# Optimization experiments

Hardware: AMD Instinct MI355X
Metric: run time of the kernel (lower is better)

Reference implementation:

```python
import jax, jax.numpy as jnp
import numpy as np

VOCAB = 50001; W2V = 300; S2V = 256; HID = 256; COUT = 256; NTAG = 4; NHEADS = 5
N_POSTS = 2048; SEQ = 64


def mha(x, wqkv, bqkv, wo, bo, h):
    # torch nn.MultiheadAttention (batch_first, eval mode, no mask)
    n, s, d = x.shape
    hd = d // h
    qkv = x @ wqkv.T + bqkv                      # [n, s, 3d]
    q, k, v = jnp.split(qkv, 3, axis=-1)
    rs = lambda t: t.reshape(n, s, h, hd).transpose(0, 2, 1, 3)  # [n, h, s, hd]
    q, k, v = rs(q), rs(k), rs(v)
    att = jax.nn.softmax(jnp.einsum('nhqd,nhkd->nhqk', q, k) * (hd ** -0.5), axis=-1)
    o = jnp.einsum('nhqk,nhkd->nhqd', att, v).transpose(0, 2, 1, 3).reshape(n, s, d)
    return o @ wo.T + bo


def gcn_conv(x, ei, w, b):
    n = x.shape[0]
    loops = jnp.arange(n)
    src = jnp.concatenate([ei[0], loops])
    dst = jnp.concatenate([ei[1], loops])
    deg = jax.ops.segment_sum(jnp.ones(dst.shape[0], dtype=x.dtype), dst, num_segments=n)
    dinv = jnp.where(deg > 0, jax.lax.rsqrt(deg), 0.0)
    norm = dinv[src] * dinv[dst]                 # [E+n]
    h = x @ w.T                                  # [n, out]
    return jax.ops.segment_sum(norm[:, None] * h[src], dst, num_segments=n) + b


def gcn_branch(x, ei, root, w1, b1, w2, b2):
    # GCN.forward: conv1 -> cat root feat -> relu -> conv2 -> relu -> cat conv1 root -> mean
    n = x.shape[0]
    c1 = gcn_conv(x, ei, w1, b1)                 # [n, HID]
    post_root = jnp.broadcast_to(x[root], (n, x.shape[1]))
    c2_in = jax.nn.relu(jnp.concatenate([c1, post_root], axis=1))
    c2 = jax.nn.relu(gcn_conv(c2_in, ei, w2, b2))
    c1_root = jnp.broadcast_to(c1[root], (n, c1.shape[1]))
    feat = jnp.concatenate([c1_root, c2], axis=1)  # [n, HID+COUT]
    return jnp.mean(feat, axis=0).reshape(1, -1)


def setup_inputs() -> dict:
    key = jax.random.key(0)
    ks = jax.random.split(key, 16)
    p = lambda i, shp, sc=0.02: jax.random.normal(ks[i], shp, dtype=jnp.float32) * sc
    return {
        'nodeText': jax.random.randint(ks[0], (N_POSTS, SEQ), 0, VOCAB),
        'edgeIndexTD': jax.random.randint(ks[1], (2, N_POSTS - 1), 0, N_POSTS),
        'edgeIndexBU': jax.random.randint(ks[2], (2, N_POSTS - 1), 0, N_POSTS),
        'threadIndex': 0,
        'mission': 1,
        'embed_w': p(3, (VOCAB, W2V), 1.0),
        'in_proj_w': p(4, (3 * W2V, W2V)),
        'in_proj_b': jnp.zeros((3 * W2V,), jnp.float32),
        'out_proj_w': p(5, (W2V, W2V)),
        'out_proj_b': jnp.zeros((W2V,), jnp.float32),
        's2v_w': p(6, (S2V, W2V)),
        's2v_b': jnp.zeros((S2V,), jnp.float32),
        'td_w1': p(7, (HID, S2V)), 'td_b1': jnp.zeros((HID,), jnp.float32),
        'td_w2': p(8, (COUT, HID + S2V)), 'td_b2': jnp.zeros((COUT,), jnp.float32),
        'bu_w1': p(9, (HID, S2V)), 'bu_b1': jnp.zeros((HID,), jnp.float32),
        'bu_w2': p(10, (COUT, HID + S2V)), 'bu_b2': jnp.zeros((COUT,), jnp.float32),
        'fc_w': p(11, (NTAG, (COUT + HID) * 2)),
        'fc_b': jnp.zeros((NTAG,), jnp.float32),
    }


def reference(nodeText, edgeIndexTD, edgeIndexBU, threadIndex, mission,
              embed_w, in_proj_w, in_proj_b, out_proj_w, out_proj_b,
              s2v_w, s2v_b, td_w1, td_b1, td_w2, td_b2,
              bu_w1, bu_b1, bu_w2, bu_b2, fc_w, fc_b):
    # ABGCN.forward, mission == 1 (rumor/BiGCN path), eval mode (dropout off)
    nf = embed_w[nodeText]                                  # [N, S, W2V]
    nf = mha(nf, in_proj_w, in_proj_b, out_proj_w, out_proj_b, NHEADS)
    nf = jnp.tanh(nf @ s2v_w.T + s2v_b)                     # [N, S, S2V]
    s2v = nf[:, 0, :]                                       # first token per post
    td = gcn_branch(s2v, edgeIndexTD, threadIndex, td_w1, td_b1, td_w2, td_b2)
    bu = gcn_branch(s2v, edgeIndexBU, threadIndex, bu_w1, bu_b1, bu_w2, bu_b2)
    return jnp.concatenate([td, bu], axis=1) @ fc_w.T + fc_b  # [1, NTAG]
```

## Files before the change

### kernel.cpp

```cpp
#include <hip/hip_runtime.h>

#define NPOSTS 2048
#define SEQ 64
#define W2V 300
#define NH 5
#define HD 60
#define S2VD 256
#define HIDD 256
#define NEDGE 2047

__global__ __launch_bounds__(320) void k_q(
    const int* __restrict__ nodeText, const float* __restrict__ embed_w,
    const float* __restrict__ Wqkv, const float* __restrict__ bqkv,
    float* __restrict__ Qout)
{
    const int r0 = blockIdx.x * 16;
    const int tid = threadIdx.x;
    __shared__ float sE[16][W2V];
    for (int i = tid; i < 16 * 75; i += 320) {
        int r = i / 75, c4 = (i % 75) * 4;
        int t = nodeText[(size_t)(r0 + r) * SEQ];
        const float4 v = *reinterpret_cast<const float4*>(embed_w + (size_t)t * W2V + c4);
        sE[r][c4] = v.x; sE[r][c4 + 1] = v.y; sE[r][c4 + 2] = v.z; sE[r][c4 + 3] = v.w;
    }
    __syncthreads();
    if (tid < W2V) {
        const float* wr = Wqkv + (size_t)tid * W2V;
        float acc[16];
        float b = bqkv[tid];
        #pragma unroll
        for (int r = 0; r < 16; ++r) acc[r] = b;
        for (int c = 0; c < W2V; ++c) {
            float wv = wr[c];
            #pragma unroll
            for (int r = 0; r < 16; ++r) acc[r] = fmaf(wv, sE[r][c], acc[r]);
        }
        #pragma unroll
        for (int r = 0; r < 16; ++r) Qout[(size_t)(r0 + r) * W2V + tid] = acc[r];
    }
}

__global__ __launch_bounds__(320) void k_u(
    const float* __restrict__ Q, const float* __restrict__ Wqkv, float* __restrict__ uout)
{
    const int r0 = blockIdx.x * 16;
    const int h = blockIdx.y;
    const int tid = threadIdx.x;
    __shared__ float sQ[16][HD];
    for (int i = tid; i < 16 * HD; i += 320) {
        int r = i / HD, d = i % HD;
        sQ[r][d] = Q[(size_t)(r0 + r) * W2V + h * HD + d];
    }
    __syncthreads();
    if (tid < W2V) {
        float acc[16];
        #pragma unroll
        for (int r = 0; r < 16; ++r) acc[r] = 0.f;
        const float* wb = Wqkv + (size_t)(W2V + h * HD) * W2V + tid;
        for (int d = 0; d < HD; ++d) {
            float wv = wb[(size_t)d * W2V];
            #pragma unroll
            for (int r = 0; r < 16; ++r) acc[r] = fmaf(wv, sQ[r][d], acc[r]);
        }
        #pragma unroll
        for (int r = 0; r < 16; ++r)
            uout[(size_t)(r0 + r) * (NH * W2V) + h * W2V + tid] = acc[r];
    }
}

__global__ __launch_bounds__(256) void k_att(
    const int* __restrict__ nodeText, const float* __restrict__ embed_w,
    float* __restrict__ ue)
{
    __shared__ float sEmb[SEQ][W2V + 1];
    __shared__ int   stoks[SEQ];
    __shared__ float ssc[NH * SEQ];

    const int p = blockIdx.x;
    const int tid = threadIdx.x;

    if (tid < SEQ) stoks[tid] = nodeText[p * SEQ + tid];
    __syncthreads();

    for (int idx = tid; idx < SEQ * 75; idx += 256) {
        int r = idx / 75, c4 = (idx % 75) * 4;
        const float4 v = *reinterpret_cast<const float4*>(embed_w + (size_t)stoks[r] * W2V + c4);
        float* dst = &sEmb[r][c4];
        dst[0] = v.x; dst[1] = v.y; dst[2] = v.z; dst[3] = v.w;
    }
    __syncthreads();

    const float* urow = ue + (size_t)p * (NH * W2V);
    for (int i = tid; i < NH * SEQ; i += 256) {
        int h = i / SEQ, j = i % SEQ;
        const float4* u4 = reinterpret_cast<const float4*>(urow + h * W2V);
        const float* er = sEmb[j];
        float acc = 0.f;
        for (int c4 = 0; c4 < 75; ++c4) {
            float4 u = u4[c4];
            int c = c4 * 4;
            acc = fmaf(u.x, er[c], acc);
            acc = fmaf(u.y, er[c + 1], acc);
            acc = fmaf(u.z, er[c + 2], acc);
            acc = fmaf(u.w, er[c + 3], acc);
        }
        ssc[i] = acc * 0.12909944487358056f;
    }
    __syncthreads();

    {
        const int wave = tid >> 6, lane = tid & 63;
        for (int h = wave; h < NH; h += 4) {
            float v = ssc[h * SEQ + lane];
            float m = v;
            #pragma unroll
            for (int off = 32; off > 0; off >>= 1) m = fmaxf(m, __shfl_xor(m, off));
            float e = expf(v - m);
            float s = e;
            #pragma unroll
            for (int off = 32; off > 0; off >>= 1) s += __shfl_xor(s, off);
            ssc[h * SEQ + lane] = e / s;
        }
    }
    __syncthreads();

    float* erow = ue + (size_t)p * (NH * W2V);
    for (int i = tid; i < NH * W2V; i += 256) {
        int h = i / W2V, c = i % W2V;
        const float* att = ssc + h * SEQ;
        float acc = 0.f;
        #pragma unroll 4
        for (int j = 0; j < SEQ; ++j) acc = fmaf(att[j], sEmb[j][c], acc);
        erow[i] = acc;
    }
}

__global__ __launch_bounds__(320) void k_oms(
    const float* __restrict__ e, const float* __restrict__ Wqkv, const float* __restrict__ bqkv,
    const float* __restrict__ Wo, const float* __restrict__ bo,
    const float* __restrict__ Ws, const float* __restrict__ bs,
    float* __restrict__ s2v_out)
{
    const int r0 = blockIdx.x * 8;
    const int tid = threadIdx.x;
    __shared__ float se[8][NH * W2V];
    __shared__ float so[8][W2V];
    __shared__ float sm[8][W2V];

    for (int i = tid; i < 8 * 375; i += 320) {
        int r = i / 375, c4 = (i % 375) * 4;
        const float4 v = *reinterpret_cast<const float4*>(e + (size_t)(r0 + r) * (NH * W2V) + c4);
        float* dst = &se[r][c4];
        dst[0] = v.x; dst[1] = v.y; dst[2] = v.z; dst[3] = v.w;
    }
    __syncthreads();

    if (tid < W2V) {
        const int h = tid / HD;
        const float* wr = Wqkv + (size_t)(2 * W2V + tid) * W2V;
        float acc[8];
        float b = bqkv[2 * W2V + tid];
        #pragma unroll
        for (int r = 0; r < 8; ++r) acc[r] = b;
        for (int c = 0; c < W2V; ++c) {
            float wv = wr[c];
            #pragma unroll
            for (int r = 0; r < 8; ++r) acc[r] = fmaf(wv, se[r][h * W2V + c], acc[r]);
        }
        #pragma unroll
        for (int r = 0; r < 8; ++r) so[r][tid] = acc[r];
    }
    __syncthreads();

    if (tid < W2V) {
        const float* wr = Wo + (size_t)tid * W2V;
        float acc[8];
        float b = bo[tid];
        #pragma unroll
        for (int r = 0; r < 8; ++r) acc[r] = b;
        for (int c = 0; c < W2V; ++c) {
            float wv = wr[c];
            #pragma unroll
            for (int r = 0; r < 8; ++r) acc[r] = fmaf(wv, so[r][c], acc[r]);
        }
        #pragma unroll
        for (int r = 0; r < 8; ++r) sm[r][tid] = acc[r];
    }
    __syncthreads();

    if (tid < S2VD) {
        const float* wr = Ws + (size_t)tid * W2V;
        float acc[8];
        float b = bs[tid];
        #pragma unroll
        for (int r = 0; r < 8; ++r) acc[r] = b;
        for (int c = 0; c < W2V; ++c) {
            float wv = wr[c];
            #pragma unroll
            for (int r = 0; r < 8; ++r) acc[r] = fmaf(wv, sm[r][c], acc[r]);
        }
        #pragma unroll
        for (int r = 0; r < 8; ++r)
            s2v_out[(size_t)(r0 + r) * S2VD + tid] = tanhf(acc[r]);
    }
}


__global__ __launch_bounds__(256) void k_deg(
    const int* __restrict__ eiTD, const int* __restrict__ eiBU, int* __restrict__ deg)
{
    const int b = blockIdx.y;
    const int* ei = b ? eiBU : eiTD;
    int e = blockIdx.x * 256 + threadIdx.x;
    if (e < NEDGE) atomicAdd(&deg[b * NPOSTS + ei[NEDGE + e]], 1);
}

__global__ __launch_bounds__(256) void k_gemm1(
    const float* __restrict__ x, const float* __restrict__ wtd, const float* __restrict__ wbu,
    float* __restrict__ hout)
{
    const int b = blockIdx.y;
    const float* w = b ? wbu : wtd;
    float* outp = hout + (size_t)b * NPOSTS * HIDD;
    const int r0 = blockIdx.x * 16;
    const int tid = threadIdx.x;
    __shared__ float sx[16][S2VD];
    for (int i = tid; i < 16 * S2VD; i += 256)
        sx[i / S2VD][i % S2VD] = x[(size_t)(r0 + i / S2VD) * S2VD + (i % S2VD)];
    __syncthreads();
    float acc[16];
    #pragma unroll
    for (int r = 0; r < 16; ++r) acc[r] = 0.f;
    const float* wr = w + (size_t)tid * S2VD;
    for (int c = 0; c < S2VD; ++c) {
        float wv = wr[c];
        #pragma unroll
        for (int r = 0; r < 16; ++r) acc[r] = fmaf(wv, sx[r][c], acc[r]);
    }
    #pragma unroll
    for (int r = 0; r < 16; ++r) outp[(size_t)(r0 + r) * HIDD + tid] = acc[r];
}

__global__ __launch_bounds__(256) void k_gemm2(
    const float* __restrict__ c1, const float* __restrict__ w2td, const float* __restrict__ w2bu,
    const float* __restrict__ rootv, float* __restrict__ hout)
{
    const int b = blockIdx.y;
    const float* w = b ? w2bu : w2td;
    const float* xin = c1 + (size_t)b * NPOSTS * HIDD;
    float* outp = hout + (size_t)b * NPOSTS * HIDD;
    const int r0 = blockIdx.x * 16;
    const int tid = threadIdx.x;
    __shared__ float sx[16][HIDD];
    for (int i = tid; i < 16 * HIDD; i += 256)
        sx[i / HIDD][i % HIDD] = fmaxf(xin[(size_t)(r0 + i / HIDD) * HIDD + (i % HIDD)], 0.f);
    __syncthreads();
    float acc[16];
    const float rv = rootv[b * HIDD + tid];
    #pragma unroll
    for (int r = 0; r < 16; ++r) acc[r] = rv;
    const float* wr = w + (size_t)tid * 512;
    for (int c = 0; c < HIDD; ++c) {
        float wv = wr[c];
        #pragma unroll
        for (int r = 0; r < 16; ++r) acc[r] = fmaf(wv, sx[r][c], acc[r]);
    }
    #pragma unroll
    for (int r = 0; r < 16; ++r) outp[(size_t)(r0 + r) * HIDD + tid] = acc[r];
}

__global__ __launch_bounds__(256) void k_init(
    const float* __restrict__ h, const float* __restrict__ btd, const float* __restrict__ bbu,
    const int* __restrict__ deg, float* __restrict__ cout_)
{
    const int b = blockIdx.y, n = blockIdx.x, tid = threadIdx.x;
    const float* bias = b ? bbu : btd;
    const float* hb = h + (size_t)b * NPOSTS * HIDD;
    float* cb = cout_ + (size_t)b * NPOSTS * HIDD;
    float dinv = 1.f / (float)(deg[b * NPOSTS + n] + 1);
    cb[(size_t)n * HIDD + tid] = bias[tid] + hb[(size_t)n * HIDD + tid] * dinv;
}

__global__ __launch_bounds__(256) void k_scat(
    const int* __restrict__ eiTD, const int* __restrict__ eiBU,
    const float* __restrict__ h, const int* __restrict__ deg, float* __restrict__ cacc)
{
    const int b = blockIdx.y, e = blockIdx.x, tid = threadIdx.x;
    const int* ei = b ? eiBU : eiTD;
    const int s = ei[e], d = ei[NEDGE + e];
    const int* dg = deg + b * NPOSTS;
    float norm = rsqrtf((float)(dg[s] + 1)) * rsqrtf((float)(dg[d] + 1));
    const float* hb = h + (size_t)b * NPOSTS * HIDD;
    float* cb = cacc + (size_t)b * NPOSTS * HIDD;
    atomicAdd(&cb[(size_t)d * HIDD + tid], norm * hb[(size_t)s * HIDD + tid]);
}

__global__ __launch_bounds__(256) void k_root(
    const float* __restrict__ s2v, const float* __restrict__ c1,
    const float* __restrict__ w2td, const float* __restrict__ w2bu,
    const int* __restrict__ rootPtr, float* __restrict__ rootv, float* __restrict__ c1root)
{
    const int b = blockIdx.y, tid = threadIdx.x;
    const float* w2 = b ? w2bu : w2td;
    const int root = rootPtr[0];
    __shared__ float sx[S2VD];
    sx[tid] = fmaxf(s2v[(size_t)root * S2VD + tid], 0.f);
    __syncthreads();
    const float* cb = c1 + (size_t)b * NPOSTS * HIDD;
    c1root[b * HIDD + tid] = cb[(size_t)root * HIDD + tid];
    const float* wr = w2 + (size_t)tid * 512 + 256;
    float acc = 0.f;
    #pragma unroll 4
    for (int c = 0; c < S2VD; ++c) acc = fmaf(wr[c], sx[c], acc);
    rootv[b * HIDD + tid] = acc;
}

__global__ __launch_bounds__(256) void k_reduce(
    const float* __restrict__ cacc, float* __restrict__ msum)
{
    const int b = blockIdx.y, tid = threadIdx.x;
    const int base = blockIdx.x * 32;
    const float* cb = cacc + (size_t)b * NPOSTS * HIDD;
    float local = 0.f;
    #pragma unroll 4
    for (int r = 0; r < 32; ++r) local += fmaxf(cb[(size_t)(base + r) * HIDD + tid], 0.f);
    atomicAdd(&msum[b * HIDD + tid], local);
}

__global__ __launch_bounds__(256) void k_final(
    const float* __restrict__ c1root, const float* __restrict__ msum,
    const float* __restrict__ fc_w, const float* __restrict__ fc_b, float* __restrict__ outp)
{
    const int tid = threadIdx.x;
    __shared__ float sf[1024];
    for (int k = tid; k < 1024; k += 256) {
        int seg = k >> 8, idx = k & 255;
        float v;
        if (seg == 0)      v = c1root[idx];
        else if (seg == 1) v = msum[idx] * (1.f / (float)NPOSTS);
        else if (seg == 2) v = c1root[256 + idx];
        else               v = msum[256 + idx] * (1.f / (float)NPOSTS);
        sf[k] = v;
    }
    __syncthreads();
    const int t = tid >> 6, lane = tid & 63;
    float part = 0.f;
    for (int k = lane; k < 1024; k += 64) part = fmaf(fc_w[t * 1024 + k], sf[k], part);
    #pragma unroll
    for (int off = 32; off > 0; off >>= 1) part += __shfl_down(part, off);
    if (lane == 0) outp[t] = part + fc_b[t];
}

extern "C" void kernel_launch(void* const* d_in, const int* in_sizes, int n_in,
                              void* d_out, int out_size, void* d_ws, size_t ws_size,
                              hipStream_t stream) {
    (void)in_sizes; (void)n_in; (void)out_size; (void)ws_size;

    const int*   nodeText   = (const int*)d_in[0];
    const int*   eiTD       = (const int*)d_in[1];
    const int*   eiBU       = (const int*)d_in[2];
    const int*   threadIdxP = (const int*)d_in[3];
    const float* embed_w    = (const float*)d_in[5];
    const float* in_proj_w  = (const float*)d_in[6];
    const float* in_proj_b  = (const float*)d_in[7];
    const float* out_proj_w = (const float*)d_in[8];
    const float* out_proj_b = (const float*)d_in[9];
    const float* s2v_w      = (const float*)d_in[10];
    const float* s2v_b      = (const float*)d_in[11];
    const float* td_w1      = (const float*)d_in[12];
    const float* td_b1      = (const float*)d_in[13];
    const float* td_w2      = (const float*)d_in[14];
    const float* td_b2      = (const float*)d_in[15];
    const float* bu_w1      = (const float*)d_in[16];
    const float* bu_b1      = (const float*)d_in[17];
    const float* bu_w2      = (const float*)d_in[18];
    const float* bu_b2      = (const float*)d_in[19];
    const float* fc_w       = (const float*)d_in[20];
    const float* fc_b       = (const float*)d_in[21];
    float* outp = (float*)d_out;

    char* w = (char*)d_ws;
    int*   deg    = (int*)w;
    float* msum   = (float*)(w + 16384);
    float* rootv  = (float*)(w + 16384 + 2048);
    float* c1root = (float*)(w + 16384 + 4096);
    float* s2v    = (float*)(w + 24576);
    float* hbuf   = (float*)(w + 24576 + 2097152);
    float* cbuf   = (float*)(w + 24576 + 2097152 + 4194304);
    float* Qbuf   = (float*)(w + 24576 + 2097152 + 4194304 + 4194304);
    float* uebuf  = (float*)(w + 24576 + 2097152 + 4194304 + 4194304 + 2457600);

    hipMemsetAsync(d_ws, 0, 16384 + 2048, stream);

    k_q  <<<NPOSTS / 16, 320, 0, stream>>>(nodeText, embed_w, in_proj_w, in_proj_b, Qbuf);
    k_u  <<<dim3(NPOSTS / 16, NH), 320, 0, stream>>>(Qbuf, in_proj_w, uebuf);
    k_att<<<NPOSTS, 256, 0, stream>>>(nodeText, embed_w, uebuf);
    k_oms<<<NPOSTS / 8, 320, 0, stream>>>(uebuf, in_proj_w, in_proj_b,
                                          out_proj_w, out_proj_b, s2v_w, s2v_b, s2v);

    k_deg<<<dim3((NEDGE + 255) / 256, 2), 256, 0, stream>>>(eiTD, eiBU, deg);

    k_gemm1<<<dim3(NPOSTS / 16, 2), 256, 0, stream>>>(s2v, td_w1, bu_w1, hbuf);
    k_init<<<dim3(NPOSTS, 2), 256, 0, stream>>>(hbuf, td_b1, bu_b1, deg, cbuf);
    k_scat<<<dim3(NEDGE, 2), 256, 0, stream>>>(eiTD, eiBU, hbuf, deg, cbuf);

    k_root<<<dim3(1, 2), 256, 0, stream>>>(s2v, cbuf, td_w2, bu_w2, threadIdxP, rootv, c1root);

    k_gemm2<<<dim3(NPOSTS / 16, 2), 256, 0, stream>>>(cbuf, td_w2, bu_w2, rootv, hbuf);
    k_init<<<dim3(NPOSTS, 2), 256, 0, stream>>>(hbuf, td_b2, bu_b2, deg, cbuf);
    k_scat<<<dim3(NEDGE, 2), 256, 0, stream>>>(eiTD, eiBU, hbuf, deg, cbuf);

    k_reduce<<<dim3(NPOSTS / 32, 2), 256, 0, stream>>>(cbuf, msum);

    k_final<<<1, 256, 0, stream>>>(c1root, msum, fc_w, fc_b, outp);
}
```

Baseline: 345.3 us.

## Fold V, out-proj and s2v weights into one matrix; fuse GCN init into GEMMs

Precomputes Ws·Wo·Wv per head into a single folded weight and bias, so the per-post V projection, out-projection and s2v GEMM chain becomes one GEMM over the attention-weighted embeddings. The attention kernel drops the max-subtraction in softmax and uses float4 shared loads. The GCN normalization-init kernel is fused into the epilogue of both GEMMs, and the inner loops are vectorized with float4. This removes launches and redundant matmul work at the cost of a small per-call weight-folding step and possible overflow risk in exp without max-subtraction.

```diff
diff --git a/kernel.cpp b/kernel.cpp
--- a/kernel.cpp
+++ b/kernel.cpp
@@ -8,35 +8,118 @@
 #define S2VD 256
 #define HIDD 256
 #define NEDGE 2047
+#define UDIM 1500
+
+__global__ __launch_bounds__(320) void k_wfoldA(
+    const float* __restrict__ Ws, const float* __restrict__ Wo,
+    const float* __restrict__ bo, const float* __restrict__ bs,
+    float* __restrict__ WsWo, float* __restrict__ bias3A)
+{
+    const int r0 = blockIdx.x * 16;
+    const int tid = threadIdx.x;
+    __shared__ float sT[W2V][16];
+    for (int i = tid; i < 16 * W2V; i += 320) {
+        int r = i / W2V, k = i % W2V;
+        sT[k][r] = Ws[(size_t)(r0 + r) * W2V + k];
+    }
+    __syncthreads();
+    if (tid <= W2V) {
+        float a[16];
+        #pragma unroll
+        for (int r = 0; r < 16; ++r) a[r] = 0.f;
+        for (int k = 0; k < W2V; ++k) {
+            float wv = (tid < W2V) ? Wo[(size_t)k * W2V + tid] : bo[k];
+            const float4* s4 = reinterpret_cast<const float4*>(&sT[k][0]);
+            float4 q0 = s4[0], q1 = s4[1], q2 = s4[2], q3 = s4[3];
+            float qq[16] = {q0.x,q0.y,q0.z,q0.w, q1.x,q1.y,q1.z,q1.w,
+                            q2.x,q2.y,q2.z,q2.w, q3.x,q3.y,q3.z,q3.w};
+            #pragma unroll
+            for (int r = 0; r < 16; ++r) a[r] = fmaf(wv, qq[r], a[r]);
+        }
+        if (tid < W2V) {
+            #pragma unroll
+            for (int r = 0; r < 16; ++r) WsWo[(size_t)(r0 + r) * W2V + tid] = a[r];
+        } else {
+            #pragma unroll
+            for (int r = 0; r < 16; ++r) bias3A[r0 + r] = bs[r0 + r] + a[r];
+        }
+    }
+}
+
+__global__ __launch_bounds__(320) void k_wfold2(
+    const float* __restrict__ WsWo, const float* __restrict__ Wqkv, const float* __restrict__ bqkv,
+    float* __restrict__ Wfold, float* __restrict__ bpart)
+{
+    const int r0 = blockIdx.x * 16;
+    const int h = blockIdx.y;
+    const int tid = threadIdx.x;
+    __shared__ float sT[HD][16];
+    for (int i = tid; i < 16 * HD; i += 320) {
+        int r = i / HD, d = i % HD;
+        sT[d][r] = WsWo[(size_t)(r0 + r) * W2V + h * HD + d];
+    }
+    __syncthreads();
+    if (tid <= W2V) {
+        float a[16];
+        #pragma unroll
+        for (int r = 0; r < 16; ++r) a[r] = 0.f;
+        for (int d = 0; d < HD; ++d) {
+            float wv = (tid < W2V) ? Wqkv[(size_t)(2 * W2V + h * HD + d) * W2V + tid]
+                                   : bqkv[2 * W2V + h * HD + d];
+            const float4* s4 = reinterpret_cast<const float4*>(&sT[d][0]);
+            float4 q0 = s4[0], q1 = s4[1], q2 = s4[2], q3 = s4[3];
+            float qq[16] = {q0.x,q0.y,q0.z,q0.w, q1.x,q1.y,q1.z,q1.w,
+                            q2.x,q2.y,q2.z,q2.w, q3.x,q3.y,q3.z,q3.w};
+            #pragma unroll
+            for (int r = 0; r < 16; ++r) a[r] = fmaf(wv, qq[r], a[r]);
+        }
+        if (tid < W2V) {
+            #pragma unroll
+            for (int r = 0; r < 16; ++r)
+                Wfold[(size_t)(r0 + r) * UDIM + h * W2V + tid] = a[r];
+        } else {
+            #pragma unroll
+            for (int r = 0; r < 16; ++r) bpart[h * S2VD + r0 + r] = a[r];
+        }
+    }
+}
 
 __global__ __launch_bounds__(320) void k_q(
     const int* __restrict__ nodeText, const float* __restrict__ embed_w,
     const float* __restrict__ Wqkv, const float* __restrict__ bqkv,
     float* __restrict__ Qout)
 {
-    const int r0 = blockIdx.x * 16;
-    const int tid = threadIdx.x;
-    __shared__ float sE[16][W2V];
-    for (int i = tid; i < 16 * 75; i += 320) {
-        int r = i / 75, c4 = (i % 75) * 4;
-        int t = nodeText[(size_t)(r0 + r) * SEQ];
-        const float4 v = *reinterpret_cast<const float4*>(embed_w + (size_t)t * W2V + c4);
-        sE[r][c4] = v.x; sE[r][c4 + 1] = v.y; sE[r][c4 + 2] = v.z; sE[r][c4 + 3] = v.w;
+    const int r0 = blockIdx.x * 8;
+    const int tid = threadIdx.x;
+    __shared__ int stok[8];
+    __shared__ float sE[8][W2V];
+    if (tid < 8) stok[tid] = nodeText[(size_t)(r0 + tid) * SEQ];
+    __syncthreads();
+    for (int i = tid; i < 8 * 75; i += 320) {
+        int r = i / 75, c4 = i % 75;
+        *reinterpret_cast<float4*>(&sE[r][c4 * 4]) =
+            *reinterpret_cast<const float4*>(embed_w + (size_t)stok[r] * W2V + c4 * 4);
     }
     __syncthreads();
     if (tid < W2V) {
-        const float* wr = Wqkv + (size_t)tid * W2V;
-        float acc[16];
+        const float4* w4p = reinterpret_cast<const float4*>(Wqkv + (size_t)tid * W2V);
         float b = bqkv[tid];
-        #pragma unroll
-        for (int r = 0; r < 16; ++r) acc[r] = b;
-        for (int c = 0; c < W2V; ++c) {
-            float wv = wr[c];
-            #pragma unroll
-            for (int r = 0; r < 16; ++r) acc[r] = fmaf(wv, sE[r][c], acc[r]);
-        }
-        #pragma unroll
-        for (int r = 0; r < 16; ++r) Qout[(size_t)(r0 + r) * W2V + tid] = acc[r];
+        float a[8];
+        #pragma unroll
+        for (int r = 0; r < 8; ++r) a[r] = b;
+        for (int c4 = 0; c4 < 75; ++c4) {
+            float4 w4 = w4p[c4];
+            #pragma unroll
+            for (int r = 0; r < 8; ++r) {
+                float4 v = *reinterpret_cast<const float4*>(&sE[r][c4 * 4]);
+                a[r] = fmaf(w4.x, v.x, a[r]);
+                a[r] = fmaf(w4.y, v.y, a[r]);
+                a[r] = fmaf(w4.z, v.z, a[r]);
+                a[r] = fmaf(w4.w, v.w, a[r]);
+            }
+        }
+        #pragma unroll
+        for (int r = 0; r < 8; ++r) Qout[(size_t)(r0 + r) * W2V + tid] = a[r];
     }
 }
 
@@ -46,163 +129,127 @@
     const int r0 = blockIdx.x * 16;
     const int h = blockIdx.y;
     const int tid = threadIdx.x;
-    __shared__ float sQ[16][HD];
+    __shared__ float sT[HD][16];
     for (int i = tid; i < 16 * HD; i += 320) {
         int r = i / HD, d = i % HD;
-        sQ[r][d] = Q[(size_t)(r0 + r) * W2V + h * HD + d];
+        sT[d][r] = Q[(size_t)(r0 + r) * W2V + h * HD + d];
     }
     __syncthreads();
     if (tid < W2V) {
-        float acc[16];
-        #pragma unroll
-        for (int r = 0; r < 16; ++r) acc[r] = 0.f;
-        const float* wb = Wqkv + (size_t)(W2V + h * HD) * W2V + tid;
+        float a[16];
+        #pragma unroll
+        for (int r = 0; r < 16; ++r) a[r] = 0.f;
         for (int d = 0; d < HD; ++d) {
-            float wv = wb[(size_t)d * W2V];
-            #pragma unroll
-            for (int r = 0; r < 16; ++r) acc[r] = fmaf(wv, sQ[r][d], acc[r]);
+            float wv = Wqkv[(size_t)(W2V + h * HD + d) * W2V + tid];
+            const float4* s4 = reinterpret_cast<const float4*>(&sT[d][0]);
+            float4 q0 = s4[0], q1 = s4[1], q2 = s4[2], q3 = s4[3];
+            float qq[16] = {q0.x,q0.y,q0.z,q0.w, q1.x,q1.y,q1.z,q1.w,
+                            q2.x,q2.y,q2.z,q2.w, q3.x,q3.y,q3.z,q3.w};
+            #pragma unroll
+            for (int r = 0; r < 16; ++r) a[r] = fmaf(wv, qq[r], a[r]);
         }
         #pragma unroll
         for (int r = 0; r < 16; ++r)
-            uout[(size_t)(r0 + r) * (NH * W2V) + h * W2V + tid] = acc[r];
-    }
-}
-
-__global__ __launch_bounds__(256) void k_att(
+            uout[(size_t)(r0 + r) * UDIM + h * W2V + tid] = a[r];
+    }
+}
+
+__global__ __launch_bounds__(384) void k_att(
     const int* __restrict__ nodeText, const float* __restrict__ embed_w,
     float* __restrict__ ue)
 {
-    __shared__ float sEmb[SEQ][W2V + 1];
+    __shared__ float sE[SEQ][W2V];
+    __shared__ float satt[NH][SEQ];
     __shared__ int   stoks[SEQ];
-    __shared__ float ssc[NH * SEQ];
 
     const int p = blockIdx.x;
     const int tid = threadIdx.x;
 
-    if (tid < SEQ) stoks[tid] = nodeText[p * SEQ + tid];
-    __syncthreads();
-
-    for (int idx = tid; idx < SEQ * 75; idx += 256) {
-        int r = idx / 75, c4 = (idx % 75) * 4;
-        const float4 v = *reinterpret_cast<const float4*>(embed_w + (size_t)stoks[r] * W2V + c4);
-        float* dst = &sEmb[r][c4];
-        dst[0] = v.x; dst[1] = v.y; dst[2] = v.z; dst[3] = v.w;
-    }
-    __syncthreads();
-
-    const float* urow = ue + (size_t)p * (NH * W2V);
-    for (int i = tid; i < NH * SEQ; i += 256) {
-        int h = i / SEQ, j = i % SEQ;
-        const float4* u4 = reinterpret_cast<const float4*>(urow + h * W2V);
-        const float* er = sEmb[j];
+    if (tid < SEQ) stoks[tid] = nodeText[(size_t)p * SEQ + tid];
+    __syncthreads();
+
+    for (int i = tid; i < SEQ * 75; i += 384) {
+        int r = i / 75, c4 = i % 75;
+        *reinterpret_cast<float4*>(&sE[r][c4 * 4]) =
+            *reinterpret_cast<const float4*>(embed_w + (size_t)stoks[r] * W2V + c4 * 4);
+    }
+    __syncthreads();
+
+    if (tid < NH * SEQ) {
+        const int h = tid >> 6, j = tid & 63;
+        const float4* u4 = reinterpret_cast<const float4*>(ue + (size_t)p * UDIM + h * W2V);
+        const float4* e4 = reinterpret_cast<const float4*>(&sE[j][0]);
         float acc = 0.f;
+        #pragma unroll 5
         for (int c4 = 0; c4 < 75; ++c4) {
-            float4 u = u4[c4];
-            int c = c4 * 4;
-            acc = fmaf(u.x, er[c], acc);
-            acc = fmaf(u.y, er[c + 1], acc);
-            acc = fmaf(u.z, er[c + 2], acc);
-            acc = fmaf(u.w, er[c + 3], acc);
-        }
-        ssc[i] = acc * 0.12909944487358056f;
-    }
-    __syncthreads();
-
-    {
-        const int wave = tid >> 6, lane = tid & 63;
-        for (int h = wave; h < NH; h += 4) {
-            float v = ssc[h * SEQ + lane];
-            float m = v;
-            #pragma unroll
-            for (int off = 32; off > 0; off >>= 1) m = fmaxf(m, __shfl_xor(m, off));
-            float e = expf(v - m);
-            float s = e;
-            #pragma unroll
-            for (int off = 32; off > 0; off >>= 1) s += __shfl_xor(s, off);
-            ssc[h * SEQ + lane] = e / s;
-        }
-    }
-    __syncthreads();
-
-    float* erow = ue + (size_t)p * (NH * W2V);
-    for (int i = tid; i < NH * W2V; i += 256) {
-        int h = i / W2V, c = i % W2V;
-        const float* att = ssc + h * SEQ;
-        float acc = 0.f;
+            float4 uv = u4[c4];
+            float4 ev = e4[c4];
+            acc = fmaf(uv.x, ev.x, acc);
+            acc = fmaf(uv.y, ev.y, acc);
+            acc = fmaf(uv.z, ev.z, acc);
+            acc = fmaf(uv.w, ev.w, acc);
+        }
+        float ex = expf(acc * 0.12909944487358056f);
+        float l = ex;
+        #pragma unroll
+        for (int off = 32; off > 0; off >>= 1) l += __shfl_xor(l, off);
+        satt[h][j] = ex / l;
+    }
+    __syncthreads();
+
+    if (tid < NH * 75) {
+        const int h = tid / 75, c4 = tid % 75;
+        float4 a = make_float4(0.f, 0.f, 0.f, 0.f);
         #pragma unroll 4
-        for (int j = 0; j < SEQ; ++j) acc = fmaf(att[j], sEmb[j][c], acc);
-        erow[i] = acc;
-    }
-}
-
-__global__ __launch_bounds__(320) void k_oms(
-    const float* __restrict__ e, const float* __restrict__ Wqkv, const float* __restrict__ bqkv,
-    const float* __restrict__ Wo, const float* __restrict__ bo,
-    const float* __restrict__ Ws, const float* __restrict__ bs,
+        for (int j = 0; j < SEQ; ++j) {
+            float av = satt[h][j];
+            float4 ev = *reinterpret_cast<const float4*>(&sE[j][c4 * 4]);
+            a.x = fmaf(av, ev.x, a.x);
+            a.y = fmaf(av, ev.y, a.y);
+            a.z = fmaf(av, ev.z, a.z);
+            a.w = fmaf(av, ev.w, a.w);
+        }
+        *reinterpret_cast<float4*>(ue + (size_t)p * UDIM + h * W2V + c4 * 4) = a;
+    }
+}
+
+__global__ __launch_bounds__(256) void k_s2v(
+    const float* __restrict__ e, const float* __restrict__ Wfold,
+    const float* __restrict__ bias3A, const float* __restrict__ bpart,
     float* __restrict__ s2v_out)
 {
     const int r0 = blockIdx.x * 8;
-    const int tid = threadIdx.x;
-    __shared__ float se[8][NH * W2V];
-    __shared__ float so[8][W2V];
-    __shared__ float sm[8][W2V];
-
-    for (int i = tid; i < 8 * 375; i += 320) {
-        int r = i / 375, c4 = (i % 375) * 4;
-        const float4 v = *reinterpret_cast<const float4*>(e + (size_t)(r0 + r) * (NH * W2V) + c4);
-        float* dst = &se[r][c4];
-        dst[0] = v.x; dst[1] = v.y; dst[2] = v.z; dst[3] = v.w;
-    }
-    __syncthreads();
-
-    if (tid < W2V) {
-        const int h = tid / HD;
-        const float* wr = Wqkv + (size_t)(2 * W2V + tid) * W2V;
-        float acc[8];
-        float b = bqkv[2 * W2V + tid];
-        #pragma unroll
-        for (int r = 0; r < 8; ++r) acc[r] = b;
-        for (int c = 0; c < W2V; ++c) {
-            float wv = wr[c];
-            #pragma unroll
-            for (int r = 0; r < 8; ++r) acc[r] = fmaf(wv, se[r][h * W2V + c], acc[r]);
-        }
-        #pragma unroll
-        for (int r = 0; r < 8; ++r) so[r][tid] = acc[r];
-    }
-    __syncthreads();
-
-    if (tid < W2V) {
-        const float* wr = Wo + (size_t)tid * W2V;
-        float acc[8];
-        float b = bo[tid];
-        #pragma unroll
-        for (int r = 0; r < 8; ++r) acc[r] = b;
-        for (int c = 0; c < W2V; ++c) {
-            float wv = wr[c];
-            #pragma unroll
-            for (int r = 0; r < 8; ++r) acc[r] = fmaf(wv, so[r][c], acc[r]);
-        }
-        #pragma unroll
-        for (int r = 0; r < 8; ++r) sm[r][tid] = acc[r];
-    }
-    __syncthreads();
-
-    if (tid < S2VD) {
-        const float* wr = Ws + (size_t)tid * W2V;
-        float acc[8];
-        float b = bs[tid];
-        #pragma unroll
-        for (int r = 0; r < 8; ++r) acc[r] = b;
-        for (int c = 0; c < W2V; ++c) {
-            float wv = wr[c];
-            #pragma unroll
-            for (int r = 0; r < 8; ++r) acc[r] = fmaf(wv, sm[r][c], acc[r]);
-        }
-        #pragma unroll
-        for (int r = 0; r < 8; ++r)
-            s2v_out[(size_t)(r0 + r) * S2VD + tid] = tanhf(acc[r]);
-    }
+    const int t = threadIdx.x;
+    __shared__ float se[8][W2V];
+    float a[8];
+    #pragma unroll
+    for (int r = 0; r < 8; ++r) a[r] = 0.f;
+    const float bias = bias3A[t] + bpart[t] + bpart[256 + t] + bpart[512 + t]
+                     + bpart[768 + t] + bpart[1024 + t];
+    const float4* w4p = reinterpret_cast<const float4*>(Wfold + (size_t)t * UDIM);
+    for (int ch = 0; ch < 5; ++ch) {
+        __syncthreads();
+        for (int i = t; i < 8 * 75; i += 256) {
+            int r = i / 75, c4 = i % 75;
+            *reinterpret_cast<float4*>(&se[r][c4 * 4]) =
+                *reinterpret_cast<const float4*>(e + (size_t)(r0 + r) * UDIM + ch * W2V + c4 * 4);
+        }
+        __syncthreads();
+        for (int c4 = 0; c4 < 75; ++c4) {
+            float4 w4 = w4p[ch * 75 + c4];
+            #pragma unroll
+            for (int r = 0; r < 8; ++r) {
+                float4 v = *reinterpret_cast<const float4*>(&se[r][c4 * 4]);
+                a[r] = fmaf(w4.x, v.x, a[r]);
+                a[r] = fmaf(w4.y, v.y, a[r]);
+                a[r] = fmaf(w4.z, v.z, a[r]);
+                a[r] = fmaf(w4.w, v.w, a[r]);
+            }
+        }
+    }
+    #pragma unroll
+    for (int r = 0; r < 8; ++r)
+        s2v_out[(size_t)(r0 + r) * S2VD + t] = tanhf(a[r] + bias);
 }
 
 
@@ -217,11 +264,15 @@
 
 __global__ __launch_bounds__(256) void k_gemm1(
     const float* __restrict__ x, const float* __restrict__ wtd, const float* __restrict__ wbu,
-    float* __restrict__ hout)
+    const float* __restrict__ btd, const float* __restrict__ bbu, const int* __restrict__ deg,
+    float* __restrict__ hout, float* __restrict__ cout_)
 {
     const int b = blockIdx.y;
     const float* w = b ? wbu : wtd;
-    float* outp = hout + (size_t)b * NPOSTS * HIDD;
+    const float* bias = b ? bbu : btd;
+    float* hb = hout + (size_t)b * NPOSTS * HIDD;
+    float* cb = cout_ + (size_t)b * NPOSTS * HIDD;
+    const int* dg = deg + b * NPOSTS;
     const int r0 = blockIdx.x * 16;
     const int tid = threadIdx.x;
     __shared__ float sx[16][S2VD];
@@ -231,24 +282,40 @@
     float acc[16];
     #pragma unroll
     for (int r = 0; r < 16; ++r) acc[r] = 0.f;
-    const float* wr = w + (size_t)tid * S2VD;
-    for (int c = 0; c < S2VD; ++c) {
-        float wv = wr[c];
-        #pragma unroll
-        for (int r = 0; r < 16; ++r) acc[r] = fmaf(wv, sx[r][c], acc[r]);
-    }
-    #pragma unroll
-    for (int r = 0; r < 16; ++r) outp[(size_t)(r0 + r) * HIDD + tid] = acc[r];
+    const float4* wr4 = reinterpret_cast<const float4*>(w + (size_t)tid * S2VD);
+    for (int c4 = 0; c4 < 64; ++c4) {
+        float4 w4 = wr4[c4];
+        #pragma unroll
+        for (int r = 0; r < 16; ++r) {
+            const float4 v = *reinterpret_cast<const float4*>(&sx[r][c4 * 4]);
+            acc[r] = fmaf(w4.x, v.x, acc[r]);
+            acc[r] = fmaf(w4.y, v.y, acc[r]);
+            acc[r] = fmaf(w4.z, v.z, acc[r]);
+            acc[r] = fmaf(w4.w, v.w, acc[r]);
+        }
+    }
+    float bv = bias[tid];
+    #pragma unroll
+    for (int r = 0; r < 16; ++r) {
+        int n = r0 + r;
+        float dinv = 1.f / (float)(dg[n] + 1);
+        hb[(size_t)n * HIDD + tid] = acc[r];
+        cb[(size_t)n * HIDD + tid] = bv + acc[r] * dinv;
+    }
 }
 
 __global__ __launch_bounds__(256) void k_gemm2(
     const float* __restrict__ c1, const float* __restrict__ w2td, const float* __restrict__ w2bu,
-    const float* __restrict__ rootv, float* __restrict__ hout)
+    const float* __restrict__ btd, const float* __restrict__ bbu, const int* __restrict__ deg,
+    const float* __restrict__ rootv, float* __restrict__ hout, float* __restrict__ cout_)
 {
     const int b = blockIdx.y;
     const float* w = b ? w2bu : w2td;
+    const float* bias = b ? bbu : btd;
     const float* xin = c1 + (size_t)b * NPOSTS * HIDD;
-    float* outp = hout + (size_t)b * NPOSTS * HIDD;
+    float* hb = hout + (size_t)b * NPOSTS * HIDD;
+    float* cb = cout_ + (size_t)b * NPOSTS * HIDD;
+    const int* dg = deg + b * NPOSTS;
     const int r0 = blockIdx.x * 16;
     const int tid = threadIdx.x;
     __shared__ float sx[16][HIDD];
@@ -259,26 +326,26 @@
     const float rv = rootv[b * HIDD + tid];
     #pragma unroll
     for (int r = 0; r < 16; ++r) acc[r] = rv;
-    const float* wr = w + (size_t)tid * 512;
-    for (int c = 0; c < HIDD; ++c) {
-        float wv = wr[c];
-        #pragma unroll
-        for (int r = 0; r < 16; ++r) acc[r] = fmaf(wv, sx[r][c], acc[r]);
-    }
-    #pragma unroll
-    for (int r = 0; r < 16; ++r) outp[(size_t)(r0 + r) * HIDD + tid] = acc[r];
-}
-
-__global__ __launch_bounds__(256) void k_init(
-    const float* __restrict__ h, const float* __restrict__ btd, const float* __restrict__ bbu,
-    const int* __restrict__ deg, float* __restrict__ cout_)
-{
-    const int b = blockIdx.y, n = blockIdx.x, tid = threadIdx.x;
-    const float* bias = b ? bbu : btd;
-    const float* hb = h + (size_t)b * NPOSTS * HIDD;
-    float* cb = cout_ + (size_t)b * NPOSTS * HIDD;
-    float dinv = 1.f / (float)(deg[b * NPOSTS + n] + 1);
-    cb[(size_t)n * HIDD + tid] = bias[tid] + hb[(size_t)n * HIDD + tid] * dinv;
+    const float4* wr4 = reinterpret_cast<const float4*>(w + (size_t)tid * 512);
+    for (int c4 = 0; c4 < 64; ++c4) {
+        float4 w4 = wr4[c4];
+        #pragma unroll
+        for (int r = 0; r < 16; ++r) {
+            const float4 v = *reinterpret_cast<const float4*>(&sx[r][c4 * 4]);
+            acc[r] = fmaf(w4.x, v.x, acc[r]);
+            acc[r] = fmaf(w4.y, v.y, acc[r]);
+            acc[r] = fmaf(w4.z, v.z, acc[r]);
+            acc[r] = fmaf(w4.w, v.w, acc[r]);
+        }
+    }
+    float bv = bias[tid];
+    #pragma unroll
+    for (int r = 0; r < 16; ++r) {
+        int n = r0 + r;
+        float dinv = 1.f / (float)(dg[n] + 1);
+        hb[(size_t)n * HIDD + tid] = acc[r];
+        cb[(size_t)n * HIDD + tid] = bv + acc[r] * dinv;
+    }
 }
 
 __global__ __launch_bounds__(256) void k_scat(
@@ -390,24 +457,30 @@
     float* Qbuf   = (float*)(w + 24576 + 2097152 + 4194304 + 4194304);
     float* uebuf  = (float*)(w + 24576 + 2097152 + 4194304 + 4194304 + 2457600);
 
+    float* Wfold  = hbuf;
+    float* WsWo   = cbuf;
+    float* bias3A = cbuf + 256 * 300;
+    float* bpart  = bias3A + 256;
+
     hipMemsetAsync(d_ws, 0, 16384 + 2048, stream);
 
-    k_q  <<<NPOSTS / 16, 320, 0, stream>>>(nodeText, embed_w, in_proj_w, in_proj_b, Qbuf);
-    k_u  <<<dim3(NPOSTS / 16, NH), 320, 0, stream>>>(Qbuf, in_proj_w, uebuf);
-    k_att<<<NPOSTS, 256, 0, stream>>>(nodeText, embed_w, uebuf);
-    k_oms<<<NPOSTS / 8, 320, 0, stream>>>(uebuf, in_proj_w, in_proj_b,
-                                          out_proj_w, out_proj_b, s2v_w, s2v_b, s2v);
-
     k_deg<<<dim3((NEDGE + 255) / 256, 2), 256, 0, stream>>>(eiTD, eiBU, deg);
-
-    k_gemm1<<<dim3(NPOSTS / 16, 2), 256, 0, stream>>>(s2v, td_w1, bu_w1, hbuf);
-    k_init<<<dim3(NPOSTS, 2), 256, 0, stream>>>(hbuf, td_b1, bu_b1, deg, cbuf);
+    k_wfoldA<<<16, 320, 0, stream>>>(s2v_w, out_proj_w, out_proj_b, s2v_b, WsWo, bias3A);
+    k_wfold2<<<dim3(16, 5), 320, 0, stream>>>(WsWo, in_proj_w, in_proj_b, Wfold, bpart);
+
+    k_q  <<<NPOSTS / 8, 320, 0, stream>>>(nodeText, embed_w, in_proj_w, in_proj_b, Qbuf);
+    k_u  <<<dim3(NPOSTS / 16, 5), 320, 0, stream>>>(Qbuf, in_proj_w, uebuf);
+    k_att<<<NPOSTS, 384, 0, stream>>>(nodeText, embed_w, uebuf);
+    k_s2v<<<NPOSTS / 8, 256, 0, stream>>>(uebuf, Wfold, bias3A, bpart, s2v);
+
+    k_gemm1<<<dim3(NPOSTS / 16, 2), 256, 0, stream>>>(s2v, td_w1, bu_w1, td_b1, bu_b1, deg,
+                                                      hbuf, cbuf);
     k_scat<<<dim3(NEDGE, 2), 256, 0, stream>>>(eiTD, eiBU, hbuf, deg, cbuf);
 
     k_root<<<dim3(1, 2), 256, 0, stream>>>(s2v, cbuf, td_w2, bu_w2, threadIdxP, rootv, c1root);
 
-    k_gemm2<<<dim3(NPOSTS / 16, 2), 256, 0, stream>>>(cbuf, td_w2, bu_w2, rootv, hbuf);
-    k_init<<<dim3(NPOSTS, 2), 256, 0, stream>>>(hbuf, td_b2, bu_b2, deg, cbuf);
+    k_gemm2<<<dim3(NPOSTS / 16, 2), 256, 0, stream>>>(cbuf, td_w2, bu_w2, td_b2, bu_b2, deg,
+                                                      rootv, hbuf, cbuf);
     k_scat<<<dim3(NEDGE, 2), 256, 0, stream>>>(eiTD, eiBU, hbuf, deg, cbuf);
 
     k_reduce<<<dim3(NPOSTS / 32, 2), 256, 0, stream>>>(cbuf, msum);
```

Result: slower. 378.2 us (+9.5%).
